# Kernel tuning notes

Measured on AMD Instinct MI355X. Metric: run time of the kernel, lower is better.

The kernel has to match this reference:

```python
import jax, jax.numpy as jnp
import numpy as np
import math

D = 2048          # embedding_size
H = 16            # nheads
HD = D // H       # head_dim
S = 2048          # seq_len
B = 2
# SwiGLU hidden per source: int(2*(4*D)/3) rounded up to multiple of 256
FF = 256 * ((int(2 * (4 * D) / 3) + 255) // 256)  # 5632
EPS = 1e-6


def pe_row(seq_len, d_model):
    # PositionalEncoding buffer, but forward uses only pe[:, seq_len-1]
    pos = float(seq_len - 1)
    div = jnp.exp(jnp.arange(0, d_model, 2, dtype=jnp.float32) * (-math.log(10000.0) / d_model))
    row = jnp.zeros((d_model,), jnp.float32)
    row = row.at[0::2].set(jnp.sin(pos * div))
    row = row.at[1::2].set(jnp.cos(pos * div))
    return row  # [D]


def rmsnorm(x, g, eps=EPS):
    xf = x.astype(jnp.float32)
    n = xf * jax.lax.rsqrt(jnp.mean(xf * xf, axis=-1, keepdims=True) + eps)
    return g * n.astype(x.dtype)


def setup_inputs() -> dict:
    key = jax.random.key(0)
    ks = jax.random.split(key, 16)
    sd = 0.02
    x = jax.random.normal(ks[0], (B, S, D), jnp.float32)
    mask = jnp.triu(jnp.ones((S, S), jnp.int32), k=1)[None, None]  # [1,1,S,S], 1 = masked
    return {
        'x': x,
        'mask': mask,
        'qkv_w': jax.random.normal(ks[1], (3 * D, D), jnp.float32) * sd,
        'qkv_b': jnp.zeros((3 * D,), jnp.float32),
        'fc_w': jax.random.normal(ks[2], (D, D), jnp.float32) * sd,
        'fc_b': jnp.zeros((D,), jnp.float32),
        'w1': jax.random.normal(ks[3], (FF, D), jnp.float32) * sd,
        'b1': jnp.zeros((FF,), jnp.float32),
        'w2': jax.random.normal(ks[4], (FF, D), jnp.float32) * sd,
        'b2': jnp.zeros((FF,), jnp.float32),
        'w3': jax.random.normal(ks[5], (D, FF), jnp.float32) * sd,
        'b3': jnp.zeros((D,), jnp.float32),
        'g_attn': jnp.ones((D,), jnp.float32),
        'g_ff': jnp.ones((D,), jnp.float32),
    }


def _block(x, mask, qkv_w, qkv_b, fc_w, fc_b, w1, b1, w2, b2, w3, b3, g_attn, g_ff):
    b, s, _ = x.shape
    # attention sublayer (pre-norm)
    h_in = rmsnorm(x, g_attn)
    qkv = h_in @ qkv_w.T + qkv_b
    xq, xk, xv = jnp.split(qkv, 3, axis=-1)
    pe = pe_row(s, D)  # single row added everywhere (faithful to source)
    xq = xq + pe
    xk = xk + pe
    q = xq.reshape(b, s, H, HD).transpose(0, 2, 1, 3)
    k = xk.reshape(b, s, H, HD).transpose(0, 2, 1, 3)
    v = xv.reshape(b, s, H, HD).transpose(0, 2, 1, 3)
    scores = jnp.einsum('bhqd,bhkd->bhqk', q, k) / math.sqrt(HD)
    scores = jnp.where(mask == 1, jnp.float32(-1e9), scores)
    attn = jax.nn.softmax(scores, axis=-1)
    out = jnp.einsum('bhqk,bhkd->bhqd', attn, v)
    out = out.transpose(0, 2, 1, 3).reshape(b, s, D)
    attn_out = out @ fc_w.T + fc_b
    h = x + attn_out
    # SwiGLU FFN sublayer (pre-norm)
    f_in = rmsnorm(h, g_ff)
    gate = jax.nn.silu(f_in @ w1.T + b1) * (f_in @ w2.T + b2)
    return h + gate @ w3.T + b3


def reference(x, mask, qkv_w, qkv_b, fc_w, fc_b, w1, b1, w2, b2, w3, b3, g_attn, g_ff):
    return _block(x, mask, qkv_w, qkv_b, fc_w, fc_b, w1, b1, w2, b2, w3, b3, g_attn, g_ff)
```

## Files before the change

### kernel.cpp

```cpp
#include <hip/hip_runtime.h>
#include <math.h>


typedef __attribute__((ext_vector_type(8))) short bf16x8;
typedef __attribute__((ext_vector_type(4))) short bf16x4;
typedef __attribute__((ext_vector_type(4))) float f32x4;

#define DEVI __device__ __forceinline__

DEVI unsigned short f2bf(float f) {
  unsigned u = __builtin_bit_cast(unsigned, f);
  u += 0x7FFFu + ((u >> 16) & 1u);
  return (unsigned short)(u >> 16);
}
DEVI float bf2f(unsigned short h) {
  unsigned u = ((unsigned)h) << 16;
  return __builtin_bit_cast(float, u);
}

#define GLL16(g, l) __builtin_amdgcn_global_load_lds( \
    (const __attribute__((address_space(1))) unsigned int*)(const void*)(g), \
    (__attribute__((address_space(3))) unsigned int*)(void*)(l), 16, 0, 0)

__global__ __launch_bounds__(256) void wconv_k(const float* __restrict__ src,
                                               unsigned short* __restrict__ dst,
                                               long n8) {
  long t = (long)blockIdx.x * 256 + threadIdx.x;
  if (t >= n8) return;
  const f32x4* s = (const f32x4*)(src + t * 8);
  f32x4 a = s[0], b = s[1];
  bf16x8 o;
#pragma unroll
  for (int j = 0; j < 4; ++j) {
    o[j]     = (short)f2bf(a[j]);
    o[4 + j] = (short)f2bf(b[j]);
  }
  *(bf16x8*)(dst + t * 8) = o;
}

__global__ void pe_k(float* __restrict__ pe) {
  int c = blockIdx.x * 256 + threadIdx.x;
  if (c >= 2048) return;
  int i2 = c & ~1;
  float div = __expf(-(float)i2 * (9.210340371976184f / 2048.0f));
  float ang = 2047.0f * div;
  pe[c] = (c & 1) ? cosf(ang) : sinf(ang);
}

__global__ __launch_bounds__(256) void rmsnorm_k(const float* __restrict__ x,
                                                 const float* __restrict__ g,
                                                 unsigned short* __restrict__ out) {
  long row = blockIdx.x;
  const float* xr = x + row * 2048;
  int tid = threadIdx.x;
  f32x4 v0 = *(const f32x4*)&xr[tid * 8];
  f32x4 v1 = *(const f32x4*)&xr[tid * 8 + 4];
  float ss = 0.f;
#pragma unroll
  for (int j = 0; j < 4; ++j) ss += v0[j] * v0[j] + v1[j] * v1[j];
#pragma unroll
  for (int m = 1; m < 64; m <<= 1) ss += __shfl_xor(ss, m, 64);
  __shared__ float red[4];
  int lane = tid & 63, wv = tid >> 6;
  if (lane == 0) red[wv] = ss;
  __syncthreads();
  float tot = red[0] + red[1] + red[2] + red[3];
  float rn = rsqrtf(tot * (1.0f / 2048.0f) + 1e-6f);
  const float* gr = g + tid * 8;
  bf16x8 o;
#pragma unroll
  for (int j = 0; j < 4; ++j) {
    o[j]     = (short)f2bf(v0[j] * rn * gr[j]);
    o[4 + j] = (short)f2bf(v1[j] * rn * gr[4 + j]);
  }
  *(bf16x8*)&out[row * 2048 + tid * 8] = o;
}

template <int EPI>
__global__ __launch_bounds__(256) void gemm_bt(const unsigned short* __restrict__ A,
                                               const unsigned short* __restrict__ W,
                                               const float* __restrict__ bias,
                                               const void* __restrict__ residv,
                                               void* __restrict__ outv,
                                               int M, int N, int K) {
  __shared__ __align__(16) unsigned short lds[2][2][128 * 32];
  const int tid  = threadIdx.x;
  const int lane = tid & 63;
  const int wv   = tid >> 6;
  const int wr   = wv >> 1;
  const int wc   = wv & 1;
  const int l15  = lane & 15;
  const int lk   = (lane >> 4) << 3;
  const long tm  = (long)blockIdx.y * 128;
  const long tn  = (long)blockIdx.x * 128;

  const int srw = tid >> 2;
  const int scc = (tid & 3) << 3;
  const unsigned short* gA = A + (tm + srw) * (long)K + scc;
  const unsigned short* gB = W + (tn + srw) * (long)K + scc;
  const long rowstep = 64L * K;

  f32x4 acc[4][4] = {};

#define STAGE(buf, k0) do {                                   \
    unsigned short* lA = &lds[buf][0][(wv * 16) * 32];        \
    unsigned short* lB = &lds[buf][1][(wv * 16) * 32];        \
    GLL16(gA + (k0), lA);                                     \
    GLL16(gA + (k0) + rowstep, lA + 64 * 32);                 \
    GLL16(gB + (k0), lB);                                     \
    GLL16(gB + (k0) + rowstep, lB + 64 * 32);                 \
  } while (0)

  const int KT = K >> 5;
  STAGE(0, 0);
  int cur = 0;
  for (int kt = 0; kt < KT; ++kt) {
    __syncthreads();
    if (kt + 1 < KT) STAGE(cur ^ 1, (long)(kt + 1) << 5);
    const unsigned short* lA = &lds[cur][0][0];
    const unsigned short* lB = &lds[cur][1][0];
    bf16x8 af[4], bfv[4];
#pragma unroll
    for (int m = 0; m < 4; ++m)
      af[m] = *(const bf16x8*)&lA[(wr * 64 + m * 16 + l15) * 32 + lk];
#pragma unroll
    for (int n = 0; n < 4; ++n)
      bfv[n] = *(const bf16x8*)&lB[(wc * 64 + n * 16 + l15) * 32 + lk];
#pragma unroll
    for (int m = 0; m < 4; ++m)
#pragma unroll
      for (int n = 0; n < 4; ++n)
        acc[m][n] = __builtin_amdgcn_mfma_f32_16x16x32_bf16(af[m], bfv[n], acc[m][n], 0, 0, 0);
    cur ^= 1;
  }
#undef STAGE

  const long row0 = tm + wr * 64 + ((lane >> 4) << 2);
  const long col0 = tn + wc * 64;
#pragma unroll
  for (int n = 0; n < 4; ++n) {
    const long col = col0 + n * 16 + l15;
    const float bv = bias[col];
#pragma unroll
    for (int m = 0; m < 4; ++m) {
      const long rw = row0 + m * 16;
#pragma unroll
      for (int j = 0; j < 4; ++j) {
        const float v = acc[m][n][j] + bv;
        const long i = (rw + j) * (long)N + col;
        if (EPI == 0) {
          ((unsigned short*)outv)[i] = f2bf(v);
        } else if (EPI == 1) {
          ((float*)outv)[i] = ((const float*)residv)[i] + v;
        } else {
          float f1 = bf2f(((const unsigned short*)residv)[i]);
          float sg = f1 / (1.0f + __expf(-f1));
          ((unsigned short*)outv)[i] = f2bf(sg * v);
        }
      }
    }
  }
}

__global__ __launch_bounds__(256) void krepack_k(const unsigned short* __restrict__ qkv,
                                                 const float* __restrict__ pe,
                                                 unsigned short* __restrict__ kpe) {
  long t = (long)blockIdx.x * 256 + threadIdx.x;
  long idx = t * 8;
  long row = idx >> 11;
  int cd  = (int)(idx & 2047);
  int h = cd >> 7, d = cd & 127;
  long b = row >> 11, s = row & 2047;
  bf16x8 v = *(const bf16x8*)&qkv[row * 6144 + 2048 + cd];
  const float* per = &pe[cd];
#pragma unroll
  for (int j = 0; j < 8; ++j)
    v[j] = (short)f2bf(bf2f((unsigned short)v[j]) + per[j]);
  *(bf16x8*)&kpe[(((b * 16 + h)) * 2048 + s) * 128 + d] = v;
}

__global__ __launch_bounds__(256) void vtrans_k(const unsigned short* __restrict__ qkv,
                                                unsigned short* __restrict__ Vt) {
  const int s0 = blockIdx.x * 64;
  const int d0 = blockIdx.y * 64;
  const int bh = blockIdx.z;
  const long b = bh >> 4;
  const int h = bh & 15;
  __shared__ unsigned short tile[64][76];
  const int t = threadIdx.x;
#pragma unroll
  for (int half = 0; half < 2; ++half) {
    int c = t + half * 256;
    int r = c >> 3;
    int cc = (c & 7) * 8;
    bf16x8 v = *(const bf16x8*)&qkv[(b * 2048 + s0 + r) * 6144 + 4096 + h * 128 + d0 + cc];
#pragma unroll
    for (int j = 0; j < 8; ++j) tile[cc + j][r] = (unsigned short)v[j];
  }
  __syncthreads();
#pragma unroll
  for (int half = 0; half < 2; ++half) {
    int c = t + half * 256;
    int dr = c >> 3;
    int sc = (c & 7) * 8;
    bf16x4 lo = *(const bf16x4*)&tile[dr][sc];
    bf16x4 hi = *(const bf16x4*)&tile[dr][sc + 4];
    bf16x8 v;
#pragma unroll
    for (int j = 0; j < 4; ++j) { v[j] = lo[j]; v[4 + j] = hi[j]; }
    *(bf16x8*)&Vt[((long)bh * 128 + d0 + dr) * 2048 + s0 + sc] = v;
  }
}

__global__ __launch_bounds__(256, 2) void fattn_k(const unsigned short* __restrict__ QKV,
                                                  const float* __restrict__ pe,
                                                  const unsigned short* __restrict__ Kp,
                                                  const unsigned short* __restrict__ Vt,
                                                  unsigned short* __restrict__ O,
                                                  int qbase) {
  const int lin = blockIdx.x;
  const int chunk = lin & 7;
  const int idx = lin >> 3;
  const int bh = chunk * 4 + (idx >> 3);
  const int qsub = idx & 7;
  const int qb = qbase + ((qsub & 1) ? (qsub >> 1) : (7 - (qsub >> 1)));
  const long b = bh >> 4;
  const int h = bh & 15;
  const int q0 = qb * 128;
  const int tid = threadIdx.x, lane = tid & 63, wv = tid >> 6;
  const int l15 = lane & 15, lg = lane >> 4;
  const int qw = q0 + wv * 32;

  __shared__ __align__(16) unsigned short Kl[2][8192];
  __shared__ __align__(16) unsigned short Vl[2][8192];
  __shared__ __align__(16) unsigned short Plds[4][32][40];

  const float scale = 0.08838834764831845f;
  const unsigned short* Qb = QKV + (b * 2048 + qw) * 6144 + h * 128;
  bf16x8 qf[2][4];
#pragma unroll
  for (int r = 0; r < 2; ++r)
#pragma unroll
    for (int kc = 0; kc < 4; ++kc) {
      bf16x8 v = *(const bf16x8*)&Qb[(r * 16 + l15) * 6144 + kc * 32 + lg * 8];
      const float* per = &pe[h * 128 + kc * 32 + lg * 8];
#pragma unroll
      for (int j = 0; j < 8; ++j)
        v[j] = (short)f2bf((bf2f((unsigned short)v[j]) + per[j]) * scale);
      qf[r][kc] = v;
    }

  const unsigned short* Kg = Kp + (long)bh * 2048 * 128;
  const unsigned short* Vg = Vt + (long)bh * 128 * 2048;

  auto stage = [&](int buf, int key0) {
#pragma unroll
    for (int ld = 0; ld < 4; ++ld) {
      int sr = wv * 16 + ld * 4 + (lane >> 4);
      int sc = ((lane & 15) << 3) ^ ((sr & 7) << 3);
      GLL16(Kg + (long)(key0 + sr) * 128 + sc, &Kl[buf][wv * 2048 + ld * 512]);
      int dr = wv * 32 + ld * 8 + (lane >> 3);
      int dc = ((lane & 7) << 3) ^ ((dr & 7) << 3);
      GLL16(Vg + (long)dr * 2048 + key0 + dc, &Vl[buf][wv * 2048 + ld * 512]);
    }
  };

  f32x4 o[2][8] = {};
  float mr[2][4], sdn[2][4];
#pragma unroll
  for (int r = 0; r < 2; ++r)
#pragma unroll
    for (int j = 0; j < 4; ++j) { mr[r][j] = -1e30f; sdn[r][j] = 0.f; }

  const int nkt = (q0 >> 6) + 2;
  stage(0, 0);
  __syncthreads();
  int cur = 0;
  for (int kt = 0; kt < nkt; ++kt) {
    const int key0 = kt << 6;
    if (kt + 1 < nkt) stage(cur ^ 1, key0 + 64);
    if (key0 <= qw + 31) {
      f32x4 s[2][4] = {};
      __builtin_amdgcn_s_setprio(1);
#pragma unroll
      for (int ks = 0; ks < 4; ++ks) {
        bf16x8 kf[4];
#pragma unroll
        for (int kc = 0; kc < 4; ++kc)
          kf[kc] = *(const bf16x8*)&Kl[cur][(ks * 16 + l15) * 128 +
                                           ((kc * 32 + lg * 8) ^ ((l15 & 7) << 3))];
#pragma unroll
        for (int r = 0; r < 2; ++r)
#pragma unroll
          for (int kc = 0; kc < 4; ++kc)
            s[r][ks] = __builtin_amdgcn_mfma_f32_16x16x32_bf16(qf[r][kc], kf[kc], s[r][ks], 0, 0, 0);
      }
      __builtin_amdgcn_s_setprio(0);
      const bool maskt = (key0 + 63 > qw);
      float pm[2][4];
#pragma unroll
      for (int r = 0; r < 2; ++r)
#pragma unroll
        for (int j = 0; j < 4; ++j) pm[r][j] = -1e30f;
#pragma unroll
      for (int r = 0; r < 2; ++r)
#pragma unroll
        for (int ks = 0; ks < 4; ++ks)
#pragma unroll
          for (int j = 0; j < 4; ++j) {
            float v = s[r][ks][j];
            if (maskt) {
              int qrow = qw + r * 16 + lg * 4 + j;
              int key  = key0 + ks * 16 + l15;
              v = (key <= qrow) ? v : -1e30f;
              s[r][ks][j] = v;
            }
            pm[r][j] = fmaxf(pm[r][j], v);
          }
#pragma unroll
      for (int msk = 1; msk < 16; msk <<= 1)
#pragma unroll
        for (int r = 0; r < 2; ++r)
#pragma unroll
          for (int j = 0; j < 4; ++j) pm[r][j] = fmaxf(pm[r][j], __shfl_xor(pm[r][j], msk, 64));
      bool grow = false;
#pragma unroll
      for (int r = 0; r < 2; ++r)
#pragma unroll
        for (int j = 0; j < 4; ++j) grow = grow || (pm[r][j] > mr[r][j] + 8.0f);
      if (__any(grow)) {
#pragma unroll
        for (int r = 0; r < 2; ++r)
#pragma unroll
          for (int j = 0; j < 4; ++j) {
            float mn = fmaxf(mr[r][j], pm[r][j]);
            float corr = __expf(mr[r][j] - mn);
            mr[r][j] = mn;
            sdn[r][j] *= corr;
#pragma unroll
            for (int nf = 0; nf < 8; ++nf) o[r][nf][j] *= corr;
          }
      }
      float ps[2][4];
#pragma unroll
      for (int r = 0; r < 2; ++r)
#pragma unroll
        for (int j = 0; j < 4; ++j) ps[r][j] = 0.f;
#pragma unroll
      for (int r = 0; r < 2; ++r)
#pragma unroll
        for (int ks = 0; ks < 4; ++ks)
#pragma unroll
          for (int j = 0; j < 4; ++j) {
            float e = __expf(s[r][ks][j] - mr[r][j]);
            s[r][ks][j] = e;
            ps[r][j] += e;
          }
#pragma unroll
      for (int msk = 1; msk < 16; msk <<= 1)
#pragma unroll
        for (int r = 0; r < 2; ++r)
#pragma unroll
          for (int j = 0; j < 4; ++j) ps[r][j] += __shfl_xor(ps[r][j], msk, 64);
#pragma unroll
      for (int r = 0; r < 2; ++r)
#pragma unroll
        for (int j = 0; j < 4; ++j) sdn[r][j] += ps[r][j];
#pragma unroll
      for (int hk = 0; hk < 2; ++hk) {
#pragma unroll
        for (int r = 0; r < 2; ++r)
#pragma unroll
          for (int ks2 = 0; ks2 < 2; ++ks2)
#pragma unroll
            for (int j = 0; j < 4; ++j)
              Plds[wv][r * 16 + lg * 4 + j][ks2 * 16 + l15] = f2bf(s[r][hk * 2 + ks2][j]);
        bf16x8 pf[2];
#pragma unroll
        for (int r = 0; r < 2; ++r) {
          bf16x4 lo = *(const bf16x4*)&Plds[wv][r * 16 + l15][lg * 8];
          bf16x4 hi = *(const bf16x4*)&Plds[wv][r * 16 + l15][lg * 8 + 4];
          bf16x8 p;
#pragma unroll
          for (int j = 0; j < 4; ++j) { p[j] = lo[j]; p[4 + j] = hi[j]; }
          pf[r] = p;
        }
        __builtin_amdgcn_s_setprio(1);
#pragma unroll
        for (int nf = 0; nf < 8; ++nf) {
          bf16x8 vf = *(const bf16x8*)&Vl[cur][(nf * 16 + l15) * 64 +
                                              ((hk * 32 + lg * 8) ^ ((l15 & 7) << 3))];
#pragma unroll
          for (int r = 0; r < 2; ++r)
            o[r][nf] = __builtin_amdgcn_mfma_f32_16x16x32_bf16(pf[r], vf, o[r][nf], 0, 0, 0);
        }
        __builtin_amdgcn_s_setprio(0);
      }
    }
    __syncthreads();
    cur ^= 1;
  }
  unsigned short* Ob = O + (b * 2048 + qw) * 2048 + h * 128;
#pragma unroll
  for (int r = 0; r < 2; ++r)
#pragma unroll
    for (int j = 0; j < 4; ++j) {
      float inv = 1.0f / sdn[r][j];
#pragma unroll
      for (int nf = 0; nf < 8; ++nf)
        Ob[(long)(r * 16 + lg * 4 + j) * 2048 + nf * 16 + l15] = f2bf(o[r][nf][j] * inv);
    }
}

extern "C" void kernel_launch(void* const* d_in, const int* in_sizes, int n_in,
                              void* d_out, int out_size, void* d_ws, size_t ws_size,
                              hipStream_t stream) {
  (void)in_sizes; (void)n_in; (void)out_size; (void)ws_size;
  const float* x    = (const float*)d_in[0];
  const float* qkvw = (const float*)d_in[2];
  const float* qkvb = (const float*)d_in[3];
  const float* fcw  = (const float*)d_in[4];
  const float* fcb  = (const float*)d_in[5];
  const float* w1   = (const float*)d_in[6];
  const float* b1   = (const float*)d_in[7];
  const float* w2   = (const float*)d_in[8];
  const float* b2   = (const float*)d_in[9];
  const float* w3   = (const float*)d_in[10];
  const float* b3   = (const float*)d_in[11];
  const float* ga   = (const float*)d_in[12];
  const float* gf   = (const float*)d_in[13];

  char* ws = (char*)d_ws;
  size_t off = 0;
  auto alloc = [&](size_t bytes) -> char* {
    char* p = ws + off;
    off = (off + bytes + 255) & ~(size_t)255;
    return p;
  };
  unsigned short* wqkv  = (unsigned short*)alloc(6144L * 2048 * 2);
  unsigned short* wfc   = (unsigned short*)alloc(2048L * 2048 * 2);
  unsigned short* w1b   = (unsigned short*)alloc(5632L * 2048 * 2);
  unsigned short* w2b   = (unsigned short*)alloc(5632L * 2048 * 2);
  unsigned short* w3b   = (unsigned short*)alloc(2048L * 5632 * 2);
  float*          pe    = (float*)alloc(2048 * 4);
  unsigned short* hin   = (unsigned short*)alloc(4096L * 2048 * 2);
  unsigned short* qkv   = (unsigned short*)alloc(4096L * 6144 * 2);
  unsigned short* kpe   = (unsigned short*)alloc(4096L * 2048 * 2);
  unsigned short* Vt    = (unsigned short*)alloc(4096L * 2048 * 2);
  unsigned short* attnb = (unsigned short*)alloc(4096L * 2048 * 2);
  float* h = (float*)d_out;

  wconv_k<<<6144, 256, 0, stream>>>(qkvw, wqkv, 6144L * 2048 / 8);
  wconv_k<<<2048, 256, 0, stream>>>(fcw,  wfc,  2048L * 2048 / 8);
  wconv_k<<<5632, 256, 0, stream>>>(w1,   w1b,  5632L * 2048 / 8);
  wconv_k<<<5632, 256, 0, stream>>>(w2,   w2b,  5632L * 2048 / 8);
  wconv_k<<<5632, 256, 0, stream>>>(w3,   w3b,  2048L * 5632 / 8);
  pe_k<<<8, 256, 0, stream>>>(pe);

  rmsnorm_k<<<4096, 256, 0, stream>>>(x, ga, hin);
  gemm_bt<0><<<dim3(48, 32), 256, 0, stream>>>(hin, wqkv, qkvb, nullptr, qkv, 4096, 6144, 2048);
  krepack_k<<<4096, 256, 0, stream>>>(qkv, pe, kpe);
  vtrans_k<<<dim3(32, 2, 32), 256, 0, stream>>>(qkv, Vt);
  fattn_k<<<dim3(256), 256, 0, stream>>>(qkv, pe, kpe, Vt, attnb, 8);
  fattn_k<<<dim3(256), 256, 0, stream>>>(qkv, pe, kpe, Vt, attnb, 0);
  gemm_bt<1><<<dim3(16, 32), 256, 0, stream>>>(attnb, wfc, fcb, x, h, 4096, 2048, 2048);

  rmsnorm_k<<<4096, 256, 0, stream>>>(h, gf, hin);
  unsigned short* a1 = qkv;
  gemm_bt<0><<<dim3(44, 32), 256, 0, stream>>>(hin, w1b, b1, nullptr, a1, 4096, 5632, 2048);
  gemm_bt<2><<<dim3(44, 32), 256, 0, stream>>>(hin, w2b, b2, a1, a1, 4096, 5632, 2048);
  gemm_bt<1><<<dim3(16, 32), 256, 0, stream>>>(a1, w3b, b3, h, d_out, 4096, 2048, 5632);
}
```

Before: 792.2 us.

## Rewrite GEMM as 512-thread 256x128 tile with 4-stage LDS pipeline

Replaces the 256-thread 128x128 double-buffered GEMM with a 512-thread kernel computing 256x128 tiles. It uses a 4-slot LDS ring with three K-steps in flight, XOR-swizzled LDS layout to avoid bank conflicts, explicit vmcnt waits and raw barriers, and raised priority around the MFMA block. Block IDs are remapped across 8 XCDs for cache locality. It aims to hide global load latency and raise MFMA utilisation, at the cost of higher LDS use and one block per CU.

```diff
diff --git a/kernel.cpp b/kernel.cpp
--- a/kernel.cpp
+++ b/kernel.cpp
@@ -77,66 +77,74 @@
 }
 
 template <int EPI>
-__global__ __launch_bounds__(256) void gemm_bt(const unsigned short* __restrict__ A,
-                                               const unsigned short* __restrict__ W,
-                                               const float* __restrict__ bias,
-                                               const void* __restrict__ residv,
-                                               void* __restrict__ outv,
-                                               int M, int N, int K) {
-  __shared__ __align__(16) unsigned short lds[2][2][128 * 32];
+__global__ __launch_bounds__(512, 1) void gemm8p(const unsigned short* __restrict__ A,
+                                                 const unsigned short* __restrict__ W,
+                                                 const float* __restrict__ bias,
+                                                 const void* __restrict__ residv,
+                                                 void* __restrict__ outv,
+                                                 int M, int N, int K, int nbx) {
+  __shared__ __align__(16) unsigned short Ab[4][8192];
+  __shared__ __align__(16) unsigned short Bb[4][4096];
   const int tid  = threadIdx.x;
   const int lane = tid & 63;
   const int wv   = tid >> 6;
-  const int wr   = wv >> 1;
-  const int wc   = wv & 1;
+  const int wm   = wv >> 1;
+  const int wn   = wv & 1;
   const int l15  = lane & 15;
-  const int lk   = (lane >> 4) << 3;
-  const long tm  = (long)blockIdx.y * 128;
-  const long tn  = (long)blockIdx.x * 128;
-
-  const int srw = tid >> 2;
-  const int scc = (tid & 3) << 3;
-  const unsigned short* gA = A + (tm + srw) * (long)K + scc;
-  const unsigned short* gB = W + (tn + srw) * (long)K + scc;
-  const long rowstep = 64L * K;
+  const int lg   = lane >> 4;
+  const int cpx = gridDim.x >> 3;
+  const int wg  = (blockIdx.x & 7) * cpx + (blockIdx.x >> 3);
+  const long tm = (long)(wg / nbx) * 256;
+  const long tn = (long)(wg % nbx) * 128;
+
+  const int q = lane >> 2;
+  const int schunk = (((lane & 3) ^ ((q >> 1) & 3)) << 3);
+  const unsigned short* srcA0 = A + (long)(tm + wv * 32 + q) * K + schunk;
+  const unsigned short* srcA1 = srcA0 + 16L * K;
+  const unsigned short* srcB  = W + (long)(tn + wv * 16 + q) * K + schunk;
+
+#define STG(slot, hh) do {                                              \
+    GLL16(srcA0 + ((long)(hh) << 5), &Ab[slot][wv * 1024]);             \
+    GLL16(srcA1 + ((long)(hh) << 5), &Ab[slot][wv * 1024 + 512]);       \
+    GLL16(srcB  + ((long)(hh) << 5), &Bb[slot][wv * 512]);              \
+  } while (0)
+
+  const int NP = K >> 5;
+  STG(0, 0); STG(1, 1); STG(2, 2);
+  asm volatile("s_waitcnt vmcnt(6)" ::: "memory");
+  __builtin_amdgcn_s_barrier();
 
   f32x4 acc[4][4] = {};
-
-#define STAGE(buf, k0) do {                                   \
-    unsigned short* lA = &lds[buf][0][(wv * 16) * 32];        \
-    unsigned short* lB = &lds[buf][1][(wv * 16) * 32];        \
-    GLL16(gA + (k0), lA);                                     \
-    GLL16(gA + (k0) + rowstep, lA + 64 * 32);                 \
-    GLL16(gB + (k0), lB);                                     \
-    GLL16(gB + (k0) + rowstep, lB + 64 * 32);                 \
-  } while (0)
-
-  const int KT = K >> 5;
-  STAGE(0, 0);
-  int cur = 0;
-  for (int kt = 0; kt < KT; ++kt) {
-    __syncthreads();
-    if (kt + 1 < KT) STAGE(cur ^ 1, (long)(kt + 1) << 5);
-    const unsigned short* lA = &lds[cur][0][0];
-    const unsigned short* lB = &lds[cur][1][0];
+  const int sw = ((lg ^ ((l15 >> 1) & 3)) << 3);
+
+  for (int h = 0; h < NP; ++h) {
+    const int slot = h & 3;
     bf16x8 af[4], bfv[4];
 #pragma unroll
     for (int m = 0; m < 4; ++m)
-      af[m] = *(const bf16x8*)&lA[(wr * 64 + m * 16 + l15) * 32 + lk];
+      af[m] = *(const bf16x8*)&Ab[slot][(wm * 64 + m * 16 + l15) * 32 + sw];
 #pragma unroll
     for (int n = 0; n < 4; ++n)
-      bfv[n] = *(const bf16x8*)&lB[(wc * 64 + n * 16 + l15) * 32 + lk];
+      bfv[n] = *(const bf16x8*)&Bb[slot][(wn * 64 + n * 16 + l15) * 32 + sw];
+    if (h + 4 <= NP) STG((h + 3) & 3, h + 3);
+    __builtin_amdgcn_s_barrier();
+    __builtin_amdgcn_s_setprio(1);
 #pragma unroll
     for (int m = 0; m < 4; ++m)
 #pragma unroll
       for (int n = 0; n < 4; ++n)
         acc[m][n] = __builtin_amdgcn_mfma_f32_16x16x32_bf16(af[m], bfv[n], acc[m][n], 0, 0, 0);
-    cur ^= 1;
-  }
-#undef STAGE
-
-  const long row0 = tm + wr * 64 + ((lane >> 4) << 2);
-  const long col0 = tn + wc * 64;
+    __builtin_amdgcn_s_setprio(0);
+    if (h + 4 <= NP)      asm volatile("s_waitcnt vmcnt(6)" ::: "memory");
+    else if (h + 3 == NP) asm volatile("s_waitcnt vmcnt(3)" ::: "memory");
+    else if (h + 2 == NP) asm volatile("s_waitcnt vmcnt(0)" ::: "memory");
+    __builtin_amdgcn_s_barrier();
+  }
+#undef STG
+  __builtin_amdgcn_sched_barrier(0);
+
+  const long row0 = tm + wm * 64 + (lg << 2);
+  const long col0 = tn + wn * 64;
 #pragma unroll
   for (int n = 0; n < 4; ++n) {
     const long col = col0 + n * 16 + l15;
@@ -458,16 +466,16 @@
   pe_k<<<8, 256, 0, stream>>>(pe);
 
   rmsnorm_k<<<4096, 256, 0, stream>>>(x, ga, hin);
-  gemm_bt<0><<<dim3(48, 32), 256, 0, stream>>>(hin, wqkv, qkvb, nullptr, qkv, 4096, 6144, 2048);
+  gemm8p<0><<<768, 512, 0, stream>>>(hin, wqkv, qkvb, nullptr, qkv, 4096, 6144, 2048, 48);
   krepack_k<<<4096, 256, 0, stream>>>(qkv, pe, kpe);
   vtrans_k<<<dim3(32, 2, 32), 256, 0, stream>>>(qkv, Vt);
   fattn_k<<<dim3(256), 256, 0, stream>>>(qkv, pe, kpe, Vt, attnb, 8);
   fattn_k<<<dim3(256), 256, 0, stream>>>(qkv, pe, kpe, Vt, attnb, 0);
-  gemm_bt<1><<<dim3(16, 32), 256, 0, stream>>>(attnb, wfc, fcb, x, h, 4096, 2048, 2048);
+  gemm8p<1><<<256, 512, 0, stream>>>(attnb, wfc, fcb, x, h, 4096, 2048, 2048, 16);
 
   rmsnorm_k<<<4096, 256, 0, stream>>>(h, gf, hin);
   unsigned short* a1 = qkv;
-  gemm_bt<0><<<dim3(44, 32), 256, 0, stream>>>(hin, w1b, b1, nullptr, a1, 4096, 5632, 2048);
-  gemm_bt<2><<<dim3(44, 32), 256, 0, stream>>>(hin, w2b, b2, a1, a1, 4096, 5632, 2048);
-  gemm_bt<1><<<dim3(16, 32), 256, 0, stream>>>(a1, w3b, b3, h, d_out, 4096, 2048, 5632);
-}
+  gemm8p<0><<<704, 512, 0, stream>>>(hin, w1b, b1, nullptr, a1, 4096, 5632, 2048, 44);
+  gemm8p<2><<<704, 512, 0, stream>>>(hin, w2b, b2, a1, a1, 4096, 5632, 2048, 44);
+  gemm8p<1><<<256, 512, 0, stream>>>(a1, w3b, b3, h, d_out, 4096, 2048, 5632, 16);
+}
```

Result: slower. 865.4 us (+9.2%).

## Triple-buffer GEMM LDS with swizzle and merge attention launches

Applied to the files above, without the earlier changes.

The GEMM moves from double to triple buffered LDS staging with a prefetch distance of two tiles. It replaces __syncthreads with explicit vmcnt waits and s_barrier, and raises wave priority around the MFMA block. LDS row chunks are XOR-swizzled to reduce bank conflicts on fragment reads. Flash attention now runs as a single 512-block launch that interleaves long and short query blocks, instead of two 256-block launches. The aim is to hide global-load latency and cut launch gaps, at the cost of more LDS per block, which may lower occupancy.

```diff
diff --git a/kernel.cpp b/kernel.cpp
--- a/kernel.cpp
+++ b/kernel.cpp
@@ -83,57 +83,63 @@
                                                const void* __restrict__ residv,
                                                void* __restrict__ outv,
                                                int M, int N, int K) {
-  __shared__ __align__(16) unsigned short lds[2][2][128 * 32];
+  __shared__ __align__(16) unsigned short Ab[3][4096];
+  __shared__ __align__(16) unsigned short Bb[3][4096];
   const int tid  = threadIdx.x;
   const int lane = tid & 63;
   const int wv   = tid >> 6;
   const int wr   = wv >> 1;
   const int wc   = wv & 1;
   const int l15  = lane & 15;
-  const int lk   = (lane >> 4) << 3;
+  const int lg   = lane >> 4;
   const long tm  = (long)blockIdx.y * 128;
   const long tn  = (long)blockIdx.x * 128;
 
   const int srw = tid >> 2;
-  const int scc = (tid & 3) << 3;
-  const unsigned short* gA = A + (tm + srw) * (long)K + scc;
-  const unsigned short* gB = W + (tn + srw) * (long)K + scc;
+  const int sch = ((tid & 3) ^ ((srw >> 1) & 3)) << 3;
+  const unsigned short* gA = A + (tm + srw) * (long)K + sch;
+  const unsigned short* gB = W + (tn + srw) * (long)K + sch;
   const long rowstep = 64L * K;
 
+#define STG(slot, kt) do {                                          \
+    GLL16(gA + ((long)(kt) << 5), &Ab[slot][wv * 512]);             \
+    GLL16(gA + rowstep + ((long)(kt) << 5), &Ab[slot][2048 + wv * 512]); \
+    GLL16(gB + ((long)(kt) << 5), &Bb[slot][wv * 512]);             \
+    GLL16(gB + rowstep + ((long)(kt) << 5), &Bb[slot][2048 + wv * 512]); \
+  } while (0)
+
+  const int KT = K >> 5;
+  STG(0, 0); STG(1, 1);
+  asm volatile("s_waitcnt vmcnt(4)" ::: "memory");
+  __builtin_amdgcn_s_barrier();
+
   f32x4 acc[4][4] = {};
-
-#define STAGE(buf, k0) do {                                   \
-    unsigned short* lA = &lds[buf][0][(wv * 16) * 32];        \
-    unsigned short* lB = &lds[buf][1][(wv * 16) * 32];        \
-    GLL16(gA + (k0), lA);                                     \
-    GLL16(gA + (k0) + rowstep, lA + 64 * 32);                 \
-    GLL16(gB + (k0), lB);                                     \
-    GLL16(gB + (k0) + rowstep, lB + 64 * 32);                 \
-  } while (0)
-
-  const int KT = K >> 5;
-  STAGE(0, 0);
-  int cur = 0;
-  for (int kt = 0; kt < KT; ++kt) {
-    __syncthreads();
-    if (kt + 1 < KT) STAGE(cur ^ 1, (long)(kt + 1) << 5);
-    const unsigned short* lA = &lds[cur][0][0];
-    const unsigned short* lB = &lds[cur][1][0];
+  const int sw = ((lg ^ ((l15 >> 1) & 3)) << 3);
+
+  for (int t = 0; t < KT; ++t) {
+    const unsigned short* lA = &Ab[t % 3][0];
+    const unsigned short* lB = &Bb[t % 3][0];
     bf16x8 af[4], bfv[4];
 #pragma unroll
     for (int m = 0; m < 4; ++m)
-      af[m] = *(const bf16x8*)&lA[(wr * 64 + m * 16 + l15) * 32 + lk];
+      af[m] = *(const bf16x8*)&lA[(wr * 64 + m * 16 + l15) * 32 + sw];
 #pragma unroll
     for (int n = 0; n < 4; ++n)
-      bfv[n] = *(const bf16x8*)&lB[(wc * 64 + n * 16 + l15) * 32 + lk];
+      bfv[n] = *(const bf16x8*)&lB[(wc * 64 + n * 16 + l15) * 32 + sw];
+    if (t + 2 < KT) STG((t + 2) % 3, t + 2);
+    __builtin_amdgcn_s_setprio(1);
 #pragma unroll
     for (int m = 0; m < 4; ++m)
 #pragma unroll
       for (int n = 0; n < 4; ++n)
         acc[m][n] = __builtin_amdgcn_mfma_f32_16x16x32_bf16(af[m], bfv[n], acc[m][n], 0, 0, 0);
-    cur ^= 1;
-  }
-#undef STAGE
+    __builtin_amdgcn_s_setprio(0);
+    if (t + 2 < KT)      asm volatile("s_waitcnt vmcnt(4)" ::: "memory");
+    else if (t + 1 < KT) asm volatile("s_waitcnt vmcnt(0)" ::: "memory");
+    __builtin_amdgcn_s_barrier();
+  }
+#undef STG
+  __builtin_amdgcn_sched_barrier(0);
 
   const long row0 = tm + wr * 64 + ((lane >> 4) << 2);
   const long col0 = tn + wc * 64;
@@ -216,14 +222,13 @@
                                                   const float* __restrict__ pe,
                                                   const unsigned short* __restrict__ Kp,
                                                   const unsigned short* __restrict__ Vt,
-                                                  unsigned short* __restrict__ O,
-                                                  int qbase) {
+                                                  unsigned short* __restrict__ O) {
   const int lin = blockIdx.x;
   const int chunk = lin & 7;
   const int idx = lin >> 3;
-  const int bh = chunk * 4 + (idx >> 3);
-  const int qsub = idx & 7;
-  const int qb = qbase + ((qsub & 1) ? (qsub >> 1) : (7 - (qsub >> 1)));
+  const int bh = chunk * 4 + (idx >> 4);
+  const int i16 = idx & 15;
+  const int qb = (i16 & 1) ? ((i16 - 1) >> 1) : (15 - (i16 >> 1));
   const long b = bh >> 4;
   const int h = bh & 15;
   const int q0 = qb * 128;
@@ -461,8 +466,7 @@
   gemm_bt<0><<<dim3(48, 32), 256, 0, stream>>>(hin, wqkv, qkvb, nullptr, qkv, 4096, 6144, 2048);
   krepack_k<<<4096, 256, 0, stream>>>(qkv, pe, kpe);
   vtrans_k<<<dim3(32, 2, 32), 256, 0, stream>>>(qkv, Vt);
-  fattn_k<<<dim3(256), 256, 0, stream>>>(qkv, pe, kpe, Vt, attnb, 8);
-  fattn_k<<<dim3(256), 256, 0, stream>>>(qkv, pe, kpe, Vt, attnb, 0);
+  fattn_k<<<dim3(512), 256, 0, stream>>>(qkv, pe, kpe, Vt, attnb);
   gemm_bt<1><<<dim3(16, 32), 256, 0, stream>>>(attnb, wfc, fcb, x, h, 4096, 2048, 2048);
 
   rmsnorm_k<<<4096, 256, 0, stream>>>(h, gf, hin);
```

New measurement: 760.3 us. 1.04x faster.
